# Performance work log

Measured on AMD Instinct MI355X. Metric: run time of the kernel, lower is better.

The kernel has to match this reference:

```python
import jax, jax.numpy as jnp
import numpy as np

N_NODES = 20000
N_EDGES = 160000
IN_DIM = 512
HID = 256
N_CLASSES = 2
NUM_GRAPHS = 16


def setup_inputs() -> dict:
    key = jax.random.key(0)
    ks = jax.random.split(key, 12)
    x = jax.random.normal(ks[0], (N_NODES, IN_DIM), dtype=jnp.float32)
    edge_index = jax.random.randint(ks[1], (2, N_EDGES), 0, N_NODES, dtype=jnp.int64)
    batch = jnp.sort(jax.random.randint(ks[2], (N_NODES,), 0, NUM_GRAPHS, dtype=jnp.int64))
    def glorot(k, shape):
        lim = float(np.sqrt(6.0 / (shape[0] + shape[1])))
        return jax.random.uniform(k, shape, jnp.float32, -lim, lim)
    return {
        "x": x,
        "edge_index": edge_index,
        "batch": batch,
        "W1n": glorot(ks[3], (IN_DIM, HID)),
        "W1s": glorot(ks[4], (IN_DIM, HID)),
        "b1": jnp.zeros((HID,), jnp.float32),
        "W2n": glorot(ks[5], (HID, HID)),
        "W2s": glorot(ks[6], (HID, HID)),
        "b2": jnp.zeros((HID,), jnp.float32),
        "fc1w": glorot(ks[7], (HID, HID // 2)),
        "fc1b": jnp.zeros((HID // 2,), jnp.float32),
        "fc2w": glorot(ks[8], (HID // 2, N_CLASSES)),
        "fc2b": jnp.zeros((N_CLASSES,), jnp.float32),
    }


def _sage_conv(x, W_nbr, W_self, b, src, dst, n_nodes):
    # mean-aggregate neighbor features (messages flow src -> dst, PyG convention)
    deg = jax.ops.segment_sum(jnp.ones(src.shape, x.dtype), dst, num_segments=n_nodes)
    deg = jnp.maximum(deg, 1.0)
    aggr = jax.ops.segment_sum(x[src], dst, num_segments=n_nodes) / deg[:, None]
    # SAGEConv: lin_l(aggr) + lin_r(x) + bias (equivalent to concat-linear)
    return aggr @ W_nbr + x @ W_self + b


def reference(x, edge_index, batch, W1n, W1s, b1, W2n, W2s, b2, fc1w, fc1b, fc2w, fc2b):
    src, dst = edge_index[0], edge_index[1]
    n = x.shape[0]
    h = jax.nn.relu(_sage_conv(x, W1n, W1s, b1, src, dst, n))
    h = jax.nn.relu(_sage_conv(h, W2n, W2s, b2, src, dst, n))
    # global_mean_pool over graph ids
    cnt = jax.ops.segment_sum(jnp.ones((n,), h.dtype), batch, num_segments=NUM_GRAPHS)
    pooled = jax.ops.segment_sum(h, batch, num_segments=NUM_GRAPHS) / jnp.maximum(cnt, 1.0)[:, None]
    out = jax.nn.relu(pooled @ fc1w + fc1b) @ fc2w + fc2b
    return out
```

## Files before the change

### kernel.cpp

```cpp
#include <hip/hip_runtime.h>
#include <hip/hip_bf16.h>


#define HID 256
#define NCOL 512

typedef __bf16 bf16x8 __attribute__((ext_vector_type(8)));
typedef float floatx4 __attribute__((ext_vector_type(4)));
typedef unsigned int u32;
typedef const u32 __attribute__((address_space(1)))* gp_t;
typedef u32 __attribute__((address_space(3)))* lp_t;

__device__ __forceinline__ ushort f2bf(float f) {
    unsigned u = __float_as_uint(f);
    u += 0x7fffu + ((u >> 16) & 1u);
    return (ushort)(u >> 16);
}
__device__ __forceinline__ float bf2f(ushort b) {
    return __uint_as_float(((unsigned)b) << 16);
}

__device__ __forceinline__ void packT_work(const float* __restrict__ Wn,
                                           const float* __restrict__ Ws,
                                           ushort* __restrict__ WT, int K, int gid) {
    if (gid >= NCOL * K) return;
    int n = gid / K, k = gid - n * K;
    float v = (n < HID) ? Wn[k * HID + n] : Ws[k * HID + (n - HID)];
    WT[gid] = f2bf(v);
}

__global__ void prep_kernel(const float* __restrict__ x, ushort* __restrict__ xb, int n4,
                            const float* __restrict__ W1n, const float* __restrict__ W1s,
                            ushort* __restrict__ w1t, int K1,
                            const float* __restrict__ W2n, const float* __restrict__ W2s,
                            ushort* __restrict__ w2t, int K2,
                            const int* __restrict__ dst, int* __restrict__ degi, int n_edges,
                            int nb_cvt, int nb_w1, int nb_w2) {
    int bx = blockIdx.x, t = threadIdx.x;
    if (bx < nb_cvt) {
        int i = bx * 256 + t;
        if (i < n4) {
            float4 v = ((const float4*)x)[i];
            ushort4 o;
            o.x = f2bf(v.x); o.y = f2bf(v.y); o.z = f2bf(v.z); o.w = f2bf(v.w);
            ((ushort4*)xb)[i] = o;
        }
    } else if (bx < nb_cvt + nb_w1) {
        packT_work(W1n, W1s, w1t, K1, (bx - nb_cvt) * 256 + t);
    } else if (bx < nb_cvt + nb_w1 + nb_w2) {
        packT_work(W2n, W2s, w2t, K2, (bx - nb_cvt - nb_w1) * 256 + t);
    } else {
        int e = (bx - nb_cvt - nb_w1 - nb_w2) * 256 + t;
        if (e < n_edges) atomicAdd(&degi[dst[e]], 1);
    }
}

__global__ __launch_bounds__(256) void psum_kernel(const int* __restrict__ degi,
                                                   int* __restrict__ partials, int n) {
    int t = threadIdx.x;
    int i = blockIdx.x * 256 + t;
    int v = (i < n) ? degi[i] : 0;
#pragma unroll
    for (int d = 1; d < 64; d <<= 1) v += __shfl_xor(v, d, 64);
    __shared__ int wsum[4];
    if ((t & 63) == 0) wsum[t >> 6] = v;
    __syncthreads();
    if (t == 0) partials[blockIdx.x] = wsum[0] + wsum[1] + wsum[2] + wsum[3];
}

__global__ __launch_bounds__(256) void scan2_kernel(const int* __restrict__ degi,
                                                    const int* __restrict__ partials,
                                                    int* __restrict__ off,
                                                    int* __restrict__ cursor, int n, int nb) {
    int t = threadIdx.x, lane = t & 63, w = t >> 6;
    int c = blockIdx.x;
    int pre = 0, tot = 0;
    for (int base = 0; base < nb; base += 64) {
        int idx = base + lane;
        int pv = (idx < nb) ? partials[idx] : 0;
        pre += (idx < c) ? pv : 0;
        tot += pv;
    }
#pragma unroll
    for (int d = 1; d < 64; d <<= 1) {
        pre += __shfl_xor(pre, d, 64);
        tot += __shfl_xor(tot, d, 64);
    }
    if (c == 0 && t == 0) off[n] = tot;
    int i = c * 256 + t;
    int v = (i < n) ? degi[i] : 0;
    int s = v;
#pragma unroll
    for (int d = 1; d < 64; d <<= 1) {
        int u = __shfl_up(s, d, 64);
        if (lane >= d) s += u;
    }
    __shared__ int wsum[4];
    if (lane == 63) wsum[w] = s;
    __syncthreads();
    int woff = 0;
    for (int k = 0; k < w; ++k) woff += wsum[k];
    int excl = pre + woff + s - v;
    if (i < n) { off[i] = excl; cursor[i] = excl; }
}

__global__ void fill_kernel(const int* __restrict__ src, const int* __restrict__ dst,
                            int* __restrict__ cursor, int* __restrict__ eidx, int n_edges) {
    int e = blockIdx.x * 256 + threadIdx.x;
    if (e < n_edges) {
        int p = atomicAdd(&cursor[dst[e]], 1);
        eidx[p] = src[e];
    }
}

__global__ __launch_bounds__(256) void gemm_mfma(const ushort* __restrict__ A,
                                                 const ushort* __restrict__ BT,
                                                 ushort* __restrict__ Y, int K, int nG) {
    int b = blockIdx.x;
    int xcd = b & 7, rest = b >> 3;
    int m = rest & 3, Ggrp = rest >> 2;
    int G = xcd + 8 * Ggrp;
    if (G >= nG) return;
    int m0 = G * 64, n0 = m * 128;

    __shared__ ushort As[2][64 * 64];
    __shared__ ushort Bs[2][128 * 64];
    int tid = threadIdx.x;
    int w = tid >> 6, lane = tid & 63;
    int quad = lane >> 4, r16 = lane & 15;
    int wm = (w >> 1) * 32, wn = (w & 1) * 64;

    int arow[2], agu[2], brow[4], bgu[4];
#pragma unroll
    for (int rr = 0; rr < 2; ++rr) {
        int idx = rr * 256 + tid;
        arow[rr] = idx >> 3;
        agu[rr] = (idx & 7) ^ (arow[rr] & 7);
    }
#pragma unroll
    for (int rr = 0; rr < 4; ++rr) {
        int idx = rr * 256 + tid;
        brow[rr] = idx >> 3;
        bgu[rr] = (idx & 7) ^ (brow[rr] & 7);
    }

    auto stage = [&](int buf, int k0) {
#pragma unroll
        for (int rr = 0; rr < 2; ++rr) {
            const ushort* ga = A + (size_t)(m0 + arow[rr]) * K + k0 + agu[rr] * 8;
            ushort* la = As[buf] + (size_t)(rr * 256 + w * 64) * 8;
            __builtin_amdgcn_global_load_lds((gp_t)(const void*)ga, (lp_t)(void*)la, 16, 0, 0);
        }
#pragma unroll
        for (int rr = 0; rr < 4; ++rr) {
            const ushort* gb = BT + (size_t)(n0 + brow[rr]) * K + k0 + bgu[rr] * 8;
            ushort* lb = Bs[buf] + (size_t)(rr * 256 + w * 64) * 8;
            __builtin_amdgcn_global_load_lds((gp_t)(const void*)gb, (lp_t)(void*)lb, 16, 0, 0);
        }
    };

    floatx4 acc[2][4];
#pragma unroll
    for (int i = 0; i < 2; ++i)
#pragma unroll
        for (int j = 0; j < 4; ++j) acc[i][j] = (floatx4){0.f, 0.f, 0.f, 0.f};

    const int nk = K >> 6;
    stage(0, 0);
    for (int t = 0; t < nk; ++t) {
        int cb = t & 1;
        __syncthreads();
        if (t + 1 < nk) stage(cb ^ 1, (t + 1) << 6);
        const ushort* Ab = As[cb];
        const ushort* Bb = Bs[cb];
#pragma unroll
        for (int s = 0; s < 2; ++s) {
            bf16x8 a[2], b2[4];
#pragma unroll
            for (int i = 0; i < 2; ++i) {
                int row = wm + i * 16 + r16;
                int au = (s * 4 + quad) ^ (row & 7);
                a[i] = *(const bf16x8*)(Ab + row * 64 + au * 8);
            }
#pragma unroll
            for (int j = 0; j < 4; ++j) {
                int row = wn + j * 16 + r16;
                int bu = (s * 4 + quad) ^ (row & 7);
                b2[j] = *(const bf16x8*)(Bb + row * 64 + bu * 8);
            }
#pragma unroll
            for (int i = 0; i < 2; ++i)
#pragma unroll
                for (int j = 0; j < 4; ++j)
                    acc[i][j] = __builtin_amdgcn_mfma_f32_16x16x32_bf16(a[i], b2[j], acc[i][j], 0, 0, 0);
        }
    }
#pragma unroll
    for (int i = 0; i < 2; ++i)
#pragma unroll
        for (int j = 0; j < 4; ++j) {
            int col = n0 + wn + j * 16 + r16;
#pragma unroll
            for (int rg = 0; rg < 4; ++rg) {
                int row = m0 + wm + i * 16 + quad * 4 + rg;
                Y[(size_t)row * NCOL + col] = f2bf(acc[i][j][rg]);
            }
        }
}

#define ACC4(A, Yv) { A.x += bf2f(Yv.x); A.y += bf2f(Yv.y); A.z += bf2f(Yv.z); A.w += bf2f(Yv.w); }
__global__ __launch_bounds__(256) void gather_kernel(const ushort* __restrict__ Y,
                                                     const int* __restrict__ off,
                                                     const int* __restrict__ eidx,
                                                     const float* __restrict__ bias,
                                                     ushort* __restrict__ h, int n_nodes) {
    int tid = threadIdx.x;
    int v = blockIdx.x * 4 + (tid >> 6);
    if (v >= n_nodes) return;
    int lane = tid & 63;
    int q4 = lane << 2;
    int e0 = off[v], e1 = off[v + 1];
    ushort4 sv = *(const ushort4*)(Y + (size_t)v * NCOL + HID + q4);
    float4 b = *(const float4*)(bias + q4);
    float4 a0 = make_float4(0.f, 0.f, 0.f, 0.f), a1 = a0, a2 = a0, a3 = a0;
    for (int base = e0; base < e1; base += 64) {
        int ecnt = min(64, e1 - base);
        int ev = (lane < ecnt) ? eidx[base + lane] : 0;
        int j = 0;
        for (; j + 8 <= ecnt; j += 8) {
            int s0 = __shfl(ev, j + 0), s1 = __shfl(ev, j + 1);
            int s2 = __shfl(ev, j + 2), s3 = __shfl(ev, j + 3);
            int s4 = __shfl(ev, j + 4), s5 = __shfl(ev, j + 5);
            int s6 = __shfl(ev, j + 6), s7 = __shfl(ev, j + 7);
            ushort4 y0 = *(const ushort4*)(Y + (size_t)s0 * NCOL + q4);
            ushort4 y1 = *(const ushort4*)(Y + (size_t)s1 * NCOL + q4);
            ushort4 y2 = *(const ushort4*)(Y + (size_t)s2 * NCOL + q4);
            ushort4 y3 = *(const ushort4*)(Y + (size_t)s3 * NCOL + q4);
            ushort4 y4 = *(const ushort4*)(Y + (size_t)s4 * NCOL + q4);
            ushort4 y5 = *(const ushort4*)(Y + (size_t)s5 * NCOL + q4);
            ushort4 y6 = *(const ushort4*)(Y + (size_t)s6 * NCOL + q4);
            ushort4 y7 = *(const ushort4*)(Y + (size_t)s7 * NCOL + q4);
            ACC4(a0, y0); ACC4(a1, y1); ACC4(a2, y2); ACC4(a3, y3);
            ACC4(a0, y4); ACC4(a1, y5); ACC4(a2, y6); ACC4(a3, y7);
        }
        for (; j < ecnt; ++j) {
            int s = __shfl(ev, j);
            ushort4 y = *(const ushort4*)(Y + (size_t)s * NCOL + q4);
            ACC4(a0, y);
        }
    }
    float invd = 1.0f / fmaxf((float)(e1 - e0), 1.0f);
    ushort4 r;
    r.x = f2bf(fmaxf((a0.x + a1.x + a2.x + a3.x) * invd + bf2f(sv.x) + b.x, 0.f));
    r.y = f2bf(fmaxf((a0.y + a1.y + a2.y + a3.y) * invd + bf2f(sv.y) + b.y, 0.f));
    r.z = f2bf(fmaxf((a0.z + a1.z + a2.z + a3.z) * invd + bf2f(sv.z) + b.z, 0.f));
    r.w = f2bf(fmaxf((a0.w + a1.w + a2.w + a3.w) * invd + bf2f(sv.w) + b.w, 0.f));
    *(ushort4*)(h + (size_t)v * HID + q4) = r;
}

__global__ void pool_kernel(const ushort* __restrict__ h, const int* __restrict__ batch,
                            float* __restrict__ pooled, float* __restrict__ cnt, int n_nodes) {
    int f = threadIdx.x;
    int v0 = blockIdx.x * 64;
    int vend = min(v0 + 64, n_nodes);
    if (v0 >= n_nodes) return;
    int cur = batch[v0];
    float acc = 0.f, ac = 0.f;
    for (int v = v0; v < vend; ++v) {
        int g = batch[v];
        if (g != cur) {
            atomicAdd(&pooled[cur * HID + f], acc);
            if (f == 0) atomicAdd(&cnt[cur], ac);
            acc = 0.f; ac = 0.f; cur = g;
        }
        acc += bf2f(h[(size_t)v * HID + f]);
        ac += 1.0f;
    }
    atomicAdd(&pooled[cur * HID + f], acc);
    if (f == 0) atomicAdd(&cnt[cur], ac);
}

__global__ void head_kernel(const float* __restrict__ pooled, const float* __restrict__ cnt,
                            const float* __restrict__ fc1w, const float* __restrict__ fc1b,
                            const float* __restrict__ fc2w, const float* __restrict__ fc2b,
                            float* __restrict__ out) {
    int g = blockIdx.x, j = threadIdx.x;
    __shared__ float p[256];
    __shared__ float hid[128];
    float inv = 1.0f / fmaxf(cnt[g], 1.0f);
    p[j] = pooled[g * HID + j] * inv;
    p[j + 128] = pooled[g * HID + 128 + j] * inv;
    __syncthreads();
    float a = fc1b[j];
    for (int f = 0; f < 256; ++f) a += p[f] * fc1w[f * 128 + j];
    hid[j] = fmaxf(a, 0.f);
    __syncthreads();
    if (j < 2) {
        float o = fc2b[j];
        for (int t = 0; t < 128; ++t) o += hid[t] * fc2w[t * 2 + j];
        out[g * 2 + j] = o;
    }
}

extern "C" void kernel_launch(void* const* d_in, const int* in_sizes, int n_in,
                              void* d_out, int out_size, void* d_ws, size_t ws_size,
                              hipStream_t stream) {
    const float* x    = (const float*)d_in[0];
    const int*   ei   = (const int*)d_in[1];
    const int*   batch= (const int*)d_in[2];
    const float* W1n  = (const float*)d_in[3];
    const float* W1s  = (const float*)d_in[4];
    const float* b1   = (const float*)d_in[5];
    const float* W2n  = (const float*)d_in[6];
    const float* W2s  = (const float*)d_in[7];
    const float* b2   = (const float*)d_in[8];
    const float* fc1w = (const float*)d_in[9];
    const float* fc1b = (const float*)d_in[10];
    const float* fc2w = (const float*)d_in[11];
    const float* fc2b = (const float*)d_in[12];
    float* out = (float*)d_out;

    const int n_nodes = in_sizes[2];
    const int n_edges = in_sizes[1] / 2;
    const int in_dim  = in_sizes[0] / n_nodes;
    const int Mpad    = (n_nodes + 63) & ~63;
    const int nb      = (n_nodes + 255) / 256;
    const int nG      = Mpad / 64;
    const int* src = ei;
    const int* dst = ei + n_edges;

    char* wsb = (char*)d_ws;
    size_t cur = 0;
    auto alloc = [&](size_t nbytes) { size_t o = cur; cur = (cur + nbytes + 255) & ~(size_t)255; return o; };
    size_t o_degi = alloc((size_t)n_nodes * 4);
    size_t o_pool = alloc((size_t)16 * HID * 4 + 16 * 4);
    size_t zero_end = cur;
    size_t o_off  = alloc((size_t)(n_nodes + 1) * 4);
    size_t o_cur  = alloc((size_t)n_nodes * 4);
    size_t o_part = alloc((size_t)nb * 4);
    size_t o_eidx = alloc((size_t)n_edges * 4);
    size_t o_w1   = alloc((size_t)NCOL * in_dim * 2);
    size_t o_w2   = alloc((size_t)NCOL * HID * 2);
    size_t o_xb   = alloc((size_t)Mpad * in_dim * 2);
    size_t o_hb   = alloc((size_t)Mpad * HID * 2);
    size_t o_y    = alloc((size_t)Mpad * NCOL * 2);
    (void)ws_size;

    int*    degi    = (int*)(wsb + o_degi);
    float*  pooled  = (float*)(wsb + o_pool);
    float*  cnt     = pooled + 16 * HID;
    int*    off     = (int*)(wsb + o_off);
    int*    cursor  = (int*)(wsb + o_cur);
    int*    partials= (int*)(wsb + o_part);
    int*    eidx    = (int*)(wsb + o_eidx);
    ushort* w1t     = (ushort*)(wsb + o_w1);
    ushort* w2t     = (ushort*)(wsb + o_w2);
    ushort* xb      = (ushort*)(wsb + o_xb);
    ushort* hb      = (ushort*)(wsb + o_hb);
    ushort* Y       = (ushort*)(wsb + o_y);

    hipMemsetAsync(wsb + o_degi, 0, zero_end - o_degi, stream);

    int n4 = n_nodes * in_dim / 4;
    int nb_cvt = (n4 + 255) / 256;
    int nb_w1  = (NCOL * in_dim + 255) / 256;
    int nb_w2  = (NCOL * HID + 255) / 256;
    int nb_deg = (n_edges + 255) / 256;
    prep_kernel<<<nb_cvt + nb_w1 + nb_w2 + nb_deg, 256, 0, stream>>>(
        x, xb, n4, W1n, W1s, w1t, in_dim, W2n, W2s, w2t, HID,
        dst, degi, n_edges, nb_cvt, nb_w1, nb_w2);

    psum_kernel<<<nb, 256, 0, stream>>>(degi, partials, n_nodes);
    scan2_kernel<<<nb, 256, 0, stream>>>(degi, partials, off, cursor, n_nodes, nb);
    fill_kernel<<<(n_edges + 255) / 256, 256, 0, stream>>>(src, dst, cursor, eidx, n_edges);

    int gemm_blocks = 8 * 4 * ((nG + 7) / 8);
    int gather_blocks = (n_nodes + 3) / 4;

    gemm_mfma<<<gemm_blocks, 256, 0, stream>>>(xb, w1t, Y, in_dim, nG);
    gather_kernel<<<gather_blocks, 256, 0, stream>>>(Y, off, eidx, b1, hb, n_nodes);

    gemm_mfma<<<gemm_blocks, 256, 0, stream>>>(hb, w2t, Y, HID, nG);
    gather_kernel<<<gather_blocks, 256, 0, stream>>>(Y, off, eidx, b2, hb, n_nodes);

    pool_kernel<<<(n_nodes + 63) / 64, 256, 0, stream>>>(hb, batch, pooled, cnt, n_nodes);
    head_kernel<<<16, 128, 0, stream>>>(pooled, cnt, fc1w, fc1b, fc2w, fc2b, out);
}
```

Before: 222.4 us.

## Split GEMM output into separate neighbor/self buffers and widen gather loads

The GEMM now writes the neighbor-projected and self-projected halves into two separate HID-wide arrays instead of one interleaved 512-wide Y. Each neighbor row then sits in a compact 512-byte span. The gather kernel splits each wavefront into two halves that handle alternate edges, uses 16-byte loads per lane, and combines the two halves with a cross-lane shuffle at the end. The aim is better cache-line use and fewer memory instructions in the bandwidth-bound gather. In exchange it adds a shuffle reduction, and only half the lanes do the final epilogue.

```diff
diff --git a/kernel.cpp b/kernel.cpp
--- a/kernel.cpp
+++ b/kernel.cpp
@@ -7,6 +7,7 @@
 
 typedef __bf16 bf16x8 __attribute__((ext_vector_type(8)));
 typedef float floatx4 __attribute__((ext_vector_type(4)));
+typedef ushort ushort8v __attribute__((ext_vector_type(8)));
 typedef unsigned int u32;
 typedef const u32 __attribute__((address_space(1)))* gp_t;
 typedef u32 __attribute__((address_space(3)))* lp_t;
@@ -115,7 +116,8 @@
 
 __global__ __launch_bounds__(256) void gemm_mfma(const ushort* __restrict__ A,
                                                  const ushort* __restrict__ BT,
-                                                 ushort* __restrict__ Y, int K, int nG) {
+                                                 ushort* __restrict__ Yn,
+                                                 ushort* __restrict__ Ys, int K, int nG) {
     int b = blockIdx.x;
     int xcd = b & 7, rest = b >> 3;
     int m = rest & 3, Ggrp = rest >> 2;
@@ -195,21 +197,28 @@
                     acc[i][j] = __builtin_amdgcn_mfma_f32_16x16x32_bf16(a[i], b2[j], acc[i][j], 0, 0, 0);
         }
     }
+    ushort* O = (m < 2) ? Yn : Ys;
+    int cb0 = (m < 2) ? n0 : (n0 - 256);
 #pragma unroll
     for (int i = 0; i < 2; ++i)
 #pragma unroll
         for (int j = 0; j < 4; ++j) {
-            int col = n0 + wn + j * 16 + r16;
+            int col = cb0 + wn + j * 16 + r16;
 #pragma unroll
             for (int rg = 0; rg < 4; ++rg) {
                 int row = m0 + wm + i * 16 + quad * 4 + rg;
-                Y[(size_t)row * NCOL + col] = f2bf(acc[i][j][rg]);
+                O[(size_t)row * HID + col] = f2bf(acc[i][j][rg]);
             }
         }
 }
 
-#define ACC4(A, Yv) { A.x += bf2f(Yv.x); A.y += bf2f(Yv.y); A.z += bf2f(Yv.z); A.w += bf2f(Yv.w); }
-__global__ __launch_bounds__(256) void gather_kernel(const ushort* __restrict__ Y,
+__device__ __forceinline__ void acc8(float* A, ushort8v y) {
+#pragma unroll
+    for (int i = 0; i < 8; ++i) A[i] += bf2f((ushort)y[i]);
+}
+
+__global__ __launch_bounds__(256) void gather_kernel(const ushort* __restrict__ Yn,
+                                                     const ushort* __restrict__ Ys,
                                                      const int* __restrict__ off,
                                                      const int* __restrict__ eidx,
                                                      const float* __restrict__ bias,
@@ -218,44 +227,61 @@
     int v = blockIdx.x * 4 + (tid >> 6);
     if (v >= n_nodes) return;
     int lane = tid & 63;
-    int q4 = lane << 2;
+    int half = lane >> 5, sub = lane & 31;
+    int c8 = sub << 3;
     int e0 = off[v], e1 = off[v + 1];
-    ushort4 sv = *(const ushort4*)(Y + (size_t)v * NCOL + HID + q4);
-    float4 b = *(const float4*)(bias + q4);
-    float4 a0 = make_float4(0.f, 0.f, 0.f, 0.f), a1 = a0, a2 = a0, a3 = a0;
+    float accA[8] = {0.f, 0.f, 0.f, 0.f, 0.f, 0.f, 0.f, 0.f};
+    float accB[8] = {0.f, 0.f, 0.f, 0.f, 0.f, 0.f, 0.f, 0.f};
     for (int base = e0; base < e1; base += 64) {
         int ecnt = min(64, e1 - base);
         int ev = (lane < ecnt) ? eidx[base + lane] : 0;
         int j = 0;
-        for (; j + 8 <= ecnt; j += 8) {
-            int s0 = __shfl(ev, j + 0), s1 = __shfl(ev, j + 1);
-            int s2 = __shfl(ev, j + 2), s3 = __shfl(ev, j + 3);
-            int s4 = __shfl(ev, j + 4), s5 = __shfl(ev, j + 5);
-            int s6 = __shfl(ev, j + 6), s7 = __shfl(ev, j + 7);
-            ushort4 y0 = *(const ushort4*)(Y + (size_t)s0 * NCOL + q4);
-            ushort4 y1 = *(const ushort4*)(Y + (size_t)s1 * NCOL + q4);
-            ushort4 y2 = *(const ushort4*)(Y + (size_t)s2 * NCOL + q4);
-            ushort4 y3 = *(const ushort4*)(Y + (size_t)s3 * NCOL + q4);
-            ushort4 y4 = *(const ushort4*)(Y + (size_t)s4 * NCOL + q4);
-            ushort4 y5 = *(const ushort4*)(Y + (size_t)s5 * NCOL + q4);
-            ushort4 y6 = *(const ushort4*)(Y + (size_t)s6 * NCOL + q4);
-            ushort4 y7 = *(const ushort4*)(Y + (size_t)s7 * NCOL + q4);
-            ACC4(a0, y0); ACC4(a1, y1); ACC4(a2, y2); ACC4(a3, y3);
-            ACC4(a0, y4); ACC4(a1, y5); ACC4(a2, y6); ACC4(a3, y7);
-        }
-        for (; j < ecnt; ++j) {
-            int s = __shfl(ev, j);
-            ushort4 y = *(const ushort4*)(Y + (size_t)s * NCOL + q4);
-            ACC4(a0, y);
-        }
-    }
-    float invd = 1.0f / fmaxf((float)(e1 - e0), 1.0f);
-    ushort4 r;
-    r.x = f2bf(fmaxf((a0.x + a1.x + a2.x + a3.x) * invd + bf2f(sv.x) + b.x, 0.f));
-    r.y = f2bf(fmaxf((a0.y + a1.y + a2.y + a3.y) * invd + bf2f(sv.y) + b.y, 0.f));
-    r.z = f2bf(fmaxf((a0.z + a1.z + a2.z + a3.z) * invd + bf2f(sv.z) + b.z, 0.f));
-    r.w = f2bf(fmaxf((a0.w + a1.w + a2.w + a3.w) * invd + bf2f(sv.w) + b.w, 0.f));
-    *(ushort4*)(h + (size_t)v * HID + q4) = r;
+        for (; j + 16 <= ecnt; j += 16) {
+            int s0 = __shfl(ev, j + 0 + half, 64);
+            int s1 = __shfl(ev, j + 2 + half, 64);
+            int s2 = __shfl(ev, j + 4 + half, 64);
+            int s3 = __shfl(ev, j + 6 + half, 64);
+            int s4 = __shfl(ev, j + 8 + half, 64);
+            int s5 = __shfl(ev, j + 10 + half, 64);
+            int s6 = __shfl(ev, j + 12 + half, 64);
+            int s7 = __shfl(ev, j + 14 + half, 64);
+            ushort8v y0 = *(const ushort8v*)(Yn + (size_t)s0 * HID + c8);
+            ushort8v y1 = *(const ushort8v*)(Yn + (size_t)s1 * HID + c8);
+            ushort8v y2 = *(const ushort8v*)(Yn + (size_t)s2 * HID + c8);
+            ushort8v y3 = *(const ushort8v*)(Yn + (size_t)s3 * HID + c8);
+            ushort8v y4 = *(const ushort8v*)(Yn + (size_t)s4 * HID + c8);
+            ushort8v y5 = *(const ushort8v*)(Yn + (size_t)s5 * HID + c8);
+            ushort8v y6 = *(const ushort8v*)(Yn + (size_t)s6 * HID + c8);
+            ushort8v y7 = *(const ushort8v*)(Yn + (size_t)s7 * HID + c8);
+            acc8(accA, y0); acc8(accB, y1); acc8(accA, y2); acc8(accB, y3);
+            acc8(accA, y4); acc8(accB, y5); acc8(accA, y6); acc8(accB, y7);
+        }
+        for (; j < ecnt; j += 2) {
+            int idx = j + half;
+            if (idx < ecnt) {
+                int s = __shfl(ev, idx, 64);
+                ushort8v y = *(const ushort8v*)(Yn + (size_t)s * HID + c8);
+                acc8(accA, y);
+            }
+        }
+    }
+#pragma unroll
+    for (int i = 0; i < 8; ++i) {
+        accA[i] += accB[i];
+        accA[i] += __shfl_xor(accA[i], 32, 64);
+    }
+    if (half == 0) {
+        ushort8v sv = *(const ushort8v*)(Ys + (size_t)v * HID + c8);
+        float bb[8];
+        *(float4*)(bb)     = *(const float4*)(bias + c8);
+        *(float4*)(bb + 4) = *(const float4*)(bias + c8 + 4);
+        float invd = 1.0f / fmaxf((float)(e1 - e0), 1.0f);
+        ushort8v r;
+#pragma unroll
+        for (int i = 0; i < 8; ++i)
+            r[i] = f2bf(fmaxf(accA[i] * invd + bf2f((ushort)sv[i]) + bb[i], 0.f));
+        *(ushort8v*)(h + (size_t)v * HID + c8) = r;
+    }
 }
 
 __global__ void pool_kernel(const ushort* __restrict__ h, const int* __restrict__ batch,
@@ -343,7 +369,8 @@
     size_t o_w2   = alloc((size_t)NCOL * HID * 2);
     size_t o_xb   = alloc((size_t)Mpad * in_dim * 2);
     size_t o_hb   = alloc((size_t)Mpad * HID * 2);
-    size_t o_y    = alloc((size_t)Mpad * NCOL * 2);
+    size_t o_yn   = alloc((size_t)Mpad * HID * 2);
+    size_t o_ys   = alloc((size_t)Mpad * HID * 2);
     (void)ws_size;
 
     int*    degi    = (int*)(wsb + o_degi);
@@ -357,7 +384,8 @@
     ushort* w2t     = (ushort*)(wsb + o_w2);
     ushort* xb      = (ushort*)(wsb + o_xb);
     ushort* hb      = (ushort*)(wsb + o_hb);
-    ushort* Y       = (ushort*)(wsb + o_y);
+    ushort* Yn      = (ushort*)(wsb + o_yn);
+    ushort* Ys      = (ushort*)(wsb + o_ys);
 
     hipMemsetAsync(wsb + o_degi, 0, zero_end - o_degi, stream);
 
@@ -377,11 +405,11 @@
     int gemm_blocks = 8 * 4 * ((nG + 7) / 8);
     int gather_blocks = (n_nodes + 3) / 4;
 
-    gemm_mfma<<<gemm_blocks, 256, 0, stream>>>(xb, w1t, Y, in_dim, nG);
-    gather_kernel<<<gather_blocks, 256, 0, stream>>>(Y, off, eidx, b1, hb, n_nodes);
-
-    gemm_mfma<<<gemm_blocks, 256, 0, stream>>>(hb, w2t, Y, HID, nG);
-    gather_kernel<<<gather_blocks, 256, 0, stream>>>(Y, off, eidx, b2, hb, n_nodes);
+    gemm_mfma<<<gemm_blocks, 256, 0, stream>>>(xb, w1t, Yn, Ys, in_dim, nG);
+    gather_kernel<<<gather_blocks, 256, 0, stream>>>(Yn, Ys, off, eidx, b1, hb, n_nodes);
+
+    gemm_mfma<<<gemm_blocks, 256, 0, stream>>>(hb, w2t, Yn, Ys, HID, nG);
+    gather_kernel<<<gather_blocks, 256, 0, stream>>>(Yn, Ys, off, eidx, b2, hb, n_nodes);
 
     pool_kernel<<<(n_nodes + 63) / 64, 256, 0, stream>>>(hb, batch, pooled, cnt, n_nodes);
     head_kernel<<<16, 128, 0, stream>>>(pooled, cnt, fc1w, fc1b, fc2w, fc2b, out);
```

New measurement: 223.7 us. No clear change (+0.6%).
